# Performance work log

Measured on AMD Instinct MI355X. Metric: run time of the kernel, lower is better.

The kernel has to match this reference:

```python
import jax, jax.numpy as jnp
import numpy as np

N = 50000
E = 800000
F_IN = 128
H = 128
OUT = 2


def _init_linear(key, fan_in, fan_out):
    kw, kb = jax.random.split(key)
    bound = 1.0 / np.sqrt(fan_in)
    W = jax.random.uniform(kw, (fan_in, fan_out), jnp.float32, -bound, bound)
    b = jax.random.uniform(kb, (fan_out,), jnp.float32, -bound, bound)
    return W, b


def setup_inputs() -> dict:
    key = jax.random.key(0)
    ks = jax.random.split(key, 8)
    x = jax.random.normal(ks[0], (N, F_IN), jnp.float32)
    edge_index = jax.random.randint(ks[1], (2, E), 0, N, jnp.int64)
    # layer 0: in=F_IN -> out=H ; MLP([2*F_IN, H, H])
    w1_0, b1_0 = _init_linear(ks[2], 2 * F_IN, H)
    w2_0, b2_0 = _init_linear(ks[3], H, H)
    # layer 1: in=H -> out=H ; MLP([2*H, H, H])
    w1_1, b1_1 = _init_linear(ks[4], 2 * H, H)
    w2_1, b2_1 = _init_linear(ks[5], H, H)
    # layer 2 (last): in=H -> out=OUT ; MLP([2*H, OUT, OUT])
    w1_2, b1_2 = _init_linear(ks[6], 2 * H, OUT)
    w2_2, b2_2 = _init_linear(ks[7], OUT, OUT)
    return {"x": x, "edge_index": edge_index,
            "w1_0": w1_0, "b1_0": b1_0, "w2_0": w2_0, "b2_0": b2_0,
            "w1_1": w1_1, "b1_1": b1_1, "w2_1": w2_1, "b2_1": b2_1,
            "w1_2": w1_2, "b1_2": b1_2, "w2_2": w2_2, "b2_2": b2_2}


def _edge_conv(x, src, dst, W1, b1, W2, b2):
    # message on edge (j->i): MLP(concat[x_i, x_j - x_i]); max-aggregate at i
    xi = x[dst]                       # [E, F]
    xj = x[src]                       # [E, F]
    feat = jnp.concatenate([xi, xj - xi], axis=-1)   # [E, 2F]
    msg = jnp.maximum(feat @ W1 + b1, 0.0) @ W2 + b2  # [E, out]
    agg = jax.ops.segment_max(msg, dst, num_segments=N)
    # nodes with no incoming edges get 0 (PyG scatter-max convention)
    return jnp.where(jnp.isneginf(agg), 0.0, agg)


def reference(x, edge_index, w1_0, b1_0, w2_0, b2_0,
              w1_1, b1_1, w2_1, b2_1, w1_2, b1_2, w2_2, b2_2):
    src = edge_index[0]
    dst = edge_index[1]
    h = _edge_conv(x, src, dst, w1_0, b1_0, w2_0, b2_0)
    h = jnp.maximum(h, 0.0)  # inter-layer ReLU (dropout skipped: eval mode)
    h = _edge_conv(h, src, dst, w1_1, b1_1, w2_1, b2_1)
    h = jnp.maximum(h, 0.0)
    out = _edge_conv(h, src, dst, w1_2, b1_2, w2_2, b2_2)  # [N, 2]
    return out
```

## Files before the change

kernel.cpp:

```cpp
#include <hip/hip_runtime.h>
#include <cstdint>
#include <cstddef>


#define KEY_NEGINF 0x007FFFFFu

typedef __attribute__((ext_vector_type(8))) short bf16x8;
typedef __attribute__((ext_vector_type(4))) float f32x4;

__device__ __forceinline__ unsigned fkey(float f) {
  unsigned u = __float_as_uint(f);
  return (u & 0x80000000u) ? ~u : (u | 0x80000000u);
}
__device__ __forceinline__ float funkey(unsigned k) {
  unsigned u = (k & 0x80000000u) ? (k & 0x7FFFFFFFu) : ~k;
  return __uint_as_float(u);
}
__device__ __forceinline__ unsigned short f2bf(float f) {
  unsigned u = __float_as_uint(f);
  unsigned r = u + 0x7FFFu + ((u >> 16) & 1u);
  return (unsigned short)(r >> 16);
}
__device__ __forceinline__ float bflo(unsigned u) { return __uint_as_float(u << 16); }
__device__ __forceinline__ float bfhi(unsigned u) { return __uint_as_float(u & 0xFFFF0000u); }
__device__ __forceinline__ unsigned pack2(unsigned a, unsigned b) {
  float lo = fmaxf(bflo(a) + bflo(b), 0.f);
  float hi = fmaxf(bfhi(a) + bfhi(b), 0.f);
  return (unsigned)f2bf(lo) | ((unsigned)f2bf(hi) << 16);
}

__global__ void build_wcat(const float* __restrict__ w1, float* __restrict__ wcat,
                           int F, int O) {
  int i = blockIdx.x * 256 + threadIdx.x;
  int total = F * O;
  if (i >= total) return;
  int k = i / O, o = i - k * O;
  float wa = w1[(size_t)k * O + o];
  float wb = w1[(size_t)(F + k) * O + o];
  wcat[(size_t)k * 2 * O + o] = wa - wb;
  wcat[(size_t)k * 2 * O + O + o] = wb;
}

__global__ void fill_u32(unsigned* __restrict__ p, unsigned v, size_t n) {
  size_t i = (size_t)blockIdx.x * blockDim.x + threadIdx.x;
  size_t stride = (size_t)gridDim.x * blockDim.x;
  for (; i < n; i += stride) p[i] = v;
}

__global__ void decode_relu(unsigned* __restrict__ p, size_t n) {
  size_t i = (size_t)blockIdx.x * blockDim.x + threadIdx.x;
  size_t stride = (size_t)gridDim.x * blockDim.x;
  float* pf = reinterpret_cast<float*>(p);
  for (; i < n; i += stride) {
    float v = funkey(p[i]);
    pf[i] = fmaxf(v, 0.0f);
  }
}

__global__ void final_out(const unsigned* __restrict__ p, float* __restrict__ out, size_t n) {
  size_t i = (size_t)blockIdx.x * blockDim.x + threadIdx.x;
  size_t stride = (size_t)gridDim.x * blockDim.x;
  for (; i < n; i += stride) {
    unsigned k = p[i];
    out[i] = (k == KEY_NEGINF) ? 0.0f : funkey(k);
  }
}

__global__ __launch_bounds__(256, 2) void node_gemm(
    const float* __restrict__ hin, const float* __restrict__ wcat,
    const float* __restrict__ bias, unsigned short* __restrict__ Abf,
    unsigned short* __restrict__ Bbf, int nNodes) {
  __shared__ float xt[64][132];
  __shared__ float wt[32][256];
  int t = threadIdx.x;
  int m_base = blockIdx.x * 64;

  {
    int r = t >> 2, q = t & 3;
    int gm = m_base + r;
    const float4* src = reinterpret_cast<const float4*>(hin + (size_t)gm * 128);
    #pragma unroll
    for (int j = 0; j < 8; ++j) {
      int c4 = q + 4 * j;
      float4 v = make_float4(0.f, 0.f, 0.f, 0.f);
      if (gm < nNodes) v = src[c4];
      *reinterpret_cast<float4*>(&xt[r][c4 * 4]) = v;
    }
  }

  float acc[8][8];
  #pragma unroll
  for (int i = 0; i < 8; ++i)
    #pragma unroll
    for (int j = 0; j < 8; ++j) acc[i][j] = 0.f;

  int m0 = (t >> 5) * 8;
  int c0 = (t & 31) * 8;

  for (int kc = 0; kc < 128; kc += 32) {
    __syncthreads();
    #pragma unroll
    for (int j = 0; j < 8; ++j) {
      int idx = t + 256 * j;
      reinterpret_cast<float4*>(&wt[0][0])[idx] =
          reinterpret_cast<const float4*>(wcat + (size_t)kc * 256)[idx];
    }
    __syncthreads();
    #pragma unroll 4
    for (int k = 0; k < 32; ++k) {
      float xv[8];
      #pragma unroll
      for (int i = 0; i < 8; ++i) xv[i] = xt[m0 + i][kc + k];
      float4 w0 = *reinterpret_cast<float4*>(&wt[k][c0]);
      float4 w1 = *reinterpret_cast<float4*>(&wt[k][c0 + 4]);
      #pragma unroll
      for (int i = 0; i < 8; ++i) {
        acc[i][0] += xv[i] * w0.x; acc[i][1] += xv[i] * w0.y;
        acc[i][2] += xv[i] * w0.z; acc[i][3] += xv[i] * w0.w;
        acc[i][4] += xv[i] * w1.x; acc[i][5] += xv[i] * w1.y;
        acc[i][6] += xv[i] * w1.z; acc[i][7] += xv[i] * w1.w;
      }
    }
  }

  bool isA = (c0 < 128);
  float bv[8];
  #pragma unroll
  for (int j = 0; j < 8; ++j) bv[j] = isA ? bias[c0 + j] : 0.f;
  #pragma unroll
  for (int i = 0; i < 8; ++i) {
    int gm = m_base + m0 + i;
    if (gm >= nNodes) continue;
    alignas(16) unsigned short ob[8];
    #pragma unroll
    for (int j = 0; j < 8; ++j) ob[j] = f2bf(acc[i][j] + bv[j]);
    unsigned short* dst = isA ? (Abf + (size_t)gm * 128 + c0)
                              : (Bbf + (size_t)gm * 128 + (c0 - 128));
    *reinterpret_cast<uint4*>(dst) = *reinterpret_cast<const uint4*>(ob);
  }
}

__global__ __launch_bounds__(256, 3) void edge_mfma(
    const unsigned short* __restrict__ Abf, const unsigned short* __restrict__ Bbf,
    const int* __restrict__ ei,
    const float* __restrict__ W2, const float* __restrict__ b2,
    unsigned* __restrict__ aggk, int E_) {
  __shared__ unsigned short hs[64 * 128];
  __shared__ unsigned short wl[128 * 128];
  __shared__ int dstl[64];
  int t = threadIdx.x;
  int e_base = blockIdx.x * 64;

  if (t < 64) dstl[t] = ei[E_ + min(e_base + t, E_ - 1)];

  {
    int r = t >> 2, q = t & 3;
    int e = min(e_base + r, E_ - 1);
    int s = ei[e];
    int d = ei[E_ + e];
    const uint4* Ar = reinterpret_cast<const uint4*>(Abf + (size_t)d * 128);
    const uint4* Br = reinterpret_cast<const uint4*>(Bbf + (size_t)s * 128);
    #pragma unroll
    for (int j = 0; j < 4; ++j) {
      int c = q + 4 * j;
      uint4 a = Ar[c], b = Br[c];
      uint4 o;
      o.x = pack2(a.x, b.x);
      o.y = pack2(a.y, b.y);
      o.z = pack2(a.z, b.z);
      o.w = pack2(a.w, b.w);
      *reinterpret_cast<uint4*>(&hs[r * 128 + ((c ^ (r & 7)) * 8)]) = o;
    }
  }
  {
    for (int ci = t; ci < 2048; ci += 256) {
      int n = ci & 127, kc = ci >> 7;
      alignas(16) unsigned short tmp[8];
      #pragma unroll
      for (int j = 0; j < 8; ++j)
        tmp[j] = f2bf(W2[(size_t)(kc * 8 + j) * 128 + n]);
      *reinterpret_cast<uint4*>(&wl[n * 128 + ((kc ^ (n & 7)) * 8)]) =
          *reinterpret_cast<const uint4*>(tmp);
    }
  }
  __syncthreads();

  int l = t & 63;
  int w = t >> 6;
  int strip = w * 16;
  int lr = l & 15, lh = l >> 4;
  int erow = strip + lh * 4;

  unsigned cur[8][4];
  #pragma unroll
  for (int nt = 0; nt < 8; ++nt) {
    int col = nt * 16 + lr;
    #pragma unroll
    for (int j = 0; j < 4; ++j)
      cur[nt][j] = aggk[(size_t)dstl[erow + j] * 128 + col];
  }

  bf16x8 af[4];
  int arow = strip + lr;
  #pragma unroll
  for (int ks = 0; ks < 4; ++ks) {
    int c = ks * 4 + lh;
    af[ks] = *reinterpret_cast<const bf16x8*>(&hs[arow * 128 + ((c ^ (arow & 7)) * 8)]);
  }

  f32x4 acc[8];
  #pragma unroll
  for (int nt = 0; nt < 8; ++nt) {
    acc[nt] = (f32x4){0.f, 0.f, 0.f, 0.f};
    int n = nt * 16 + lr;
    #pragma unroll
    for (int ks = 0; ks < 4; ++ks) {
      int c = ks * 4 + lh;
      bf16x8 bf = *reinterpret_cast<const bf16x8*>(&wl[n * 128 + ((c ^ (n & 7)) * 8)]);
      acc[nt] = __builtin_amdgcn_mfma_f32_16x16x32_bf16(af[ks], bf, acc[nt], 0, 0, 0);
    }
  }

  #pragma unroll
  for (int nt = 0; nt < 8; ++nt) {
    int col = nt * 16 + lr;
    float bb = b2[col];
    #pragma unroll
    for (int j = 0; j < 4; ++j) {
      unsigned key = fkey(acc[nt][j] + bb);
      if (key > cur[nt][j])
        atomicMax(aggk + (size_t)dstl[erow + j] * 128 + col, key);
    }
  }
}

__global__ void node_thin(const float* __restrict__ hin, const float* __restrict__ wcat2,
                          const float* __restrict__ b1, float* __restrict__ AB2,
                          int nNodes) {
  __shared__ float w[128 * 4];
  int t = threadIdx.x;
  if (t < 128) *reinterpret_cast<float4*>(&w[t * 4]) =
      reinterpret_cast<const float4*>(wcat2)[t];
  __syncthreads();
  int node = blockIdx.x * 64 + (t >> 2);
  int o = t & 3;
  if (node >= nNodes) return;
  const float4* h4 = reinterpret_cast<const float4*>(hin + (size_t)node * 128);
  float acc = 0.f;
  #pragma unroll 8
  for (int kk = 0; kk < 32; ++kk) {
    float4 x = h4[kk];
    acc += x.x * w[(kk * 4 + 0) * 4 + o];
    acc += x.y * w[(kk * 4 + 1) * 4 + o];
    acc += x.z * w[(kk * 4 + 2) * 4 + o];
    acc += x.w * w[(kk * 4 + 3) * 4 + o];
  }
  if (o < 2) acc += b1[o];
  AB2[(size_t)node * 4 + o] = acc;
}

__global__ void edge_small(const float* __restrict__ AB2, const int* __restrict__ ei,
                           const float* __restrict__ w2, const float* __restrict__ b2,
                           unsigned* __restrict__ aggk2, int E_) {
  int e = blockIdx.x * 256 + threadIdx.x;
  if (e >= E_) return;
  int s = ei[e];
  int d = ei[E_ + e];
  float2 a = *reinterpret_cast<const float2*>(AB2 + (size_t)d * 4);
  float2 b = *reinterpret_cast<const float2*>(AB2 + (size_t)s * 4 + 2);
  float h0 = fmaxf(a.x + b.x, 0.f);
  float h1 = fmaxf(a.y + b.y, 0.f);
  float m0 = h0 * w2[0] + h1 * w2[2] + b2[0];
  float m1 = h0 * w2[1] + h1 * w2[3] + b2[1];
  atomicMax(aggk2 + (size_t)d * 2 + 0, fkey(m0));
  atomicMax(aggk2 + (size_t)d * 2 + 1, fkey(m1));
}

extern "C" void kernel_launch(void* const* d_in, const int* in_sizes, int n_in,
                              void* d_out, int out_size, void* d_ws, size_t ws_size,
                              hipStream_t stream) {
  const float* x    = (const float*)d_in[0];
  const int*   ei   = (const int*)d_in[1];
  const float* w1_0 = (const float*)d_in[2];
  const float* b1_0 = (const float*)d_in[3];
  const float* w2_0 = (const float*)d_in[4];
  const float* b2_0 = (const float*)d_in[5];
  const float* w1_1 = (const float*)d_in[6];
  const float* b1_1 = (const float*)d_in[7];
  const float* w2_1 = (const float*)d_in[8];
  const float* b2_1 = (const float*)d_in[9];
  const float* w1_2 = (const float*)d_in[10];
  const float* b1_2 = (const float*)d_in[11];
  const float* w2_2 = (const float*)d_in[12];
  const float* b2_2 = (const float*)d_in[13];

  const int N = in_sizes[0] / 128;
  const int E = in_sizes[1] / 2;

  char* ws = (char*)d_ws;
  const size_t NB = (size_t)N * 128 * 4;
  const size_t HB = (size_t)N * 128 * 2;
  unsigned*       Z    = (unsigned*)(ws);
  unsigned short* Abf  = (unsigned short*)(ws + NB);
  unsigned short* Bbf  = (unsigned short*)(ws + NB + HB);
  float*    AB2  = (float*)(ws + NB + 2 * HB);
  unsigned* agg2 = (unsigned*)(ws + NB + 2 * HB + (size_t)N * 16);
  float*    wc0  = (float*)(ws + NB + 2 * HB + (size_t)N * 16 + (size_t)N * 8);
  float*    wc1  = wc0 + 128 * 256;
  float*    wc2  = wc1 + 128 * 256;

  const int nb = (N + 63) / 64;
  const int eb = (E + 63) / 64;
  const size_t nH = (size_t)N * 128;

  build_wcat<<<64, 256, 0, stream>>>(w1_0, wc0, 128, 128);
  build_wcat<<<64, 256, 0, stream>>>(w1_1, wc1, 128, 128);
  build_wcat<<<1, 256, 0, stream>>>(w1_2, wc2, 128, 2);

  node_gemm<<<nb, 256, 0, stream>>>(x, wc0, b1_0, Abf, Bbf, N);
  fill_u32<<<1024, 256, 0, stream>>>(Z, KEY_NEGINF, nH);
  edge_mfma<<<eb, 256, 0, stream>>>(Abf, Bbf, ei, w2_0, b2_0, Z, E);
  decode_relu<<<1024, 256, 0, stream>>>(Z, nH);

  node_gemm<<<nb, 256, 0, stream>>>((const float*)Z, wc1, b1_1, Abf, Bbf, N);
  fill_u32<<<1024, 256, 0, stream>>>(Z, KEY_NEGINF, nH);
  edge_mfma<<<eb, 256, 0, stream>>>(Abf, Bbf, ei, w2_1, b2_1, Z, E);
  decode_relu<<<1024, 256, 0, stream>>>(Z, nH);

  node_thin<<<nb, 256, 0, stream>>>((const float*)Z, wc2, b1_2, AB2, N);
  fill_u32<<<256, 256, 0, stream>>>(agg2, KEY_NEGINF, (size_t)N * 2);
  edge_small<<<(E + 255) / 256, 256, 0, stream>>>(AB2, ei, w2_2, b2_2, agg2, E);
  final_out<<<((size_t)N * 2 + 255) / 256, 256, 0, stream>>>(agg2, (float*)d_out, (size_t)N * 2);
}
```

Measured before the change: 865.3 us.

## Use MFMA node GEMM, persistent prefetching edge kernel, fold decode into consumers

The FP32 node GEMM is replaced with a bf16 MFMA kernel whose weights are pre-converted and pre-swizzled once. The decode_relu passes are removed: the node kernels now decode the order-preserving keys and apply ReLU as they load. The edge kernel becomes persistent over a capped grid. It prefetches the next tile's gathered rows into registers while the current tile computes, and it loads W2 already in bf16 instead of converting it in every block. The aim is less FP32 ALU time, fewer full-array passes and fewer per-block weight conversions, at the cost of bf16 rounding on the node GEMM inputs and more register pressure in the edge kernel.

```diff
diff --git a/kernel.cpp b/kernel.cpp
--- a/kernel.cpp
+++ b/kernel.cpp
@@ -27,6 +27,34 @@
   float lo = fmaxf(bflo(a) + bflo(b), 0.f);
   float hi = fmaxf(bfhi(a) + bfhi(b), 0.f);
   return (unsigned)f2bf(lo) | ((unsigned)f2bf(hi) << 16);
+}
+
+__global__ void build_wcatbf(const float* __restrict__ w1, unsigned short* __restrict__ wcg) {
+  int i = blockIdx.x * 256 + threadIdx.x;
+  if (i >= 256 * 16) return;
+  int n = i >> 4, c = i & 15;
+  alignas(16) unsigned short ob[8];
+  #pragma unroll
+  for (int j = 0; j < 8; ++j) {
+    int k = c * 8 + j;
+    float v;
+    if (n < 128) v = w1[(size_t)k * 128 + n] - w1[(size_t)(128 + k) * 128 + n];
+    else         v = w1[(size_t)(128 + k) * 128 + (n - 128)];
+    ob[j] = f2bf(v);
+  }
+  *reinterpret_cast<uint4*>(&wcg[n * 128 + ((c ^ (n & 7)) * 8)]) =
+      *reinterpret_cast<const uint4*>(ob);
+}
+
+__global__ void build_w2bf(const float* __restrict__ w2, unsigned short* __restrict__ wlg) {
+  int i = blockIdx.x * 256 + threadIdx.x;
+  if (i >= 128 * 16) return;
+  int n = i >> 4, c = i & 15;
+  alignas(16) unsigned short ob[8];
+  #pragma unroll
+  for (int j = 0; j < 8; ++j) ob[j] = f2bf(w2[(size_t)(c * 8 + j) * 128 + n]);
+  *reinterpret_cast<uint4*>(&wlg[n * 128 + ((c ^ (n & 7)) * 8)]) =
+      *reinterpret_cast<const uint4*>(ob);
 }
 
 __global__ void build_wcat(const float* __restrict__ w1, float* __restrict__ wcat,
@@ -47,16 +75,6 @@
   for (; i < n; i += stride) p[i] = v;
 }
 
-__global__ void decode_relu(unsigned* __restrict__ p, size_t n) {
-  size_t i = (size_t)blockIdx.x * blockDim.x + threadIdx.x;
-  size_t stride = (size_t)gridDim.x * blockDim.x;
-  float* pf = reinterpret_cast<float*>(p);
-  for (; i < n; i += stride) {
-    float v = funkey(p[i]);
-    pf[i] = fmaxf(v, 0.0f);
-  }
-}
-
 __global__ void final_out(const unsigned* __restrict__ p, float* __restrict__ out, size_t n) {
   size_t i = (size_t)blockIdx.x * blockDim.x + threadIdx.x;
   size_t stride = (size_t)gridDim.x * blockDim.x;
@@ -66,175 +84,173 @@
   }
 }
 
-__global__ __launch_bounds__(256, 2) void node_gemm(
-    const float* __restrict__ hin, const float* __restrict__ wcat,
-    const float* __restrict__ bias, unsigned short* __restrict__ Abf,
-    unsigned short* __restrict__ Bbf, int nNodes) {
-  __shared__ float xt[64][132];
-  __shared__ float wt[32][256];
+__global__ __launch_bounds__(256, 2) void node_mfma(
+    const unsigned* __restrict__ hin, int decode,
+    const unsigned short* __restrict__ wcg, const float* __restrict__ b1,
+    unsigned short* __restrict__ Abf, unsigned short* __restrict__ Bbf, int nN) {
+  __shared__ unsigned short at[64 * 128];
+  __shared__ unsigned short wt[256 * 128];
   int t = threadIdx.x;
+  {
+    const uint4* src = reinterpret_cast<const uint4*>(wcg);
+    uint4* dst = reinterpret_cast<uint4*>(wt);
+    for (int i = t; i < 4096; i += 256) dst[i] = src[i];
+  }
   int m_base = blockIdx.x * 64;
-
   {
     int r = t >> 2, q = t & 3;
-    int gm = m_base + r;
-    const float4* src = reinterpret_cast<const float4*>(hin + (size_t)gm * 128);
-    #pragma unroll
-    for (int j = 0; j < 8; ++j) {
-      int c4 = q + 4 * j;
-      float4 v = make_float4(0.f, 0.f, 0.f, 0.f);
-      if (gm < nNodes) v = src[c4];
-      *reinterpret_cast<float4*>(&xt[r][c4 * 4]) = v;
-    }
-  }
-
-  float acc[8][8];
-  #pragma unroll
-  for (int i = 0; i < 8; ++i)
-    #pragma unroll
-    for (int j = 0; j < 8; ++j) acc[i][j] = 0.f;
-
-  int m0 = (t >> 5) * 8;
-  int c0 = (t & 31) * 8;
-
-  for (int kc = 0; kc < 128; kc += 32) {
-    __syncthreads();
-    #pragma unroll
-    for (int j = 0; j < 8; ++j) {
-      int idx = t + 256 * j;
-      reinterpret_cast<float4*>(&wt[0][0])[idx] =
-          reinterpret_cast<const float4*>(wcat + (size_t)kc * 256)[idx];
-    }
-    __syncthreads();
-    #pragma unroll 4
-    for (int k = 0; k < 32; ++k) {
-      float xv[8];
-      #pragma unroll
-      for (int i = 0; i < 8; ++i) xv[i] = xt[m0 + i][kc + k];
-      float4 w0 = *reinterpret_cast<float4*>(&wt[k][c0]);
-      float4 w1 = *reinterpret_cast<float4*>(&wt[k][c0 + 4]);
-      #pragma unroll
-      for (int i = 0; i < 8; ++i) {
-        acc[i][0] += xv[i] * w0.x; acc[i][1] += xv[i] * w0.y;
-        acc[i][2] += xv[i] * w0.z; acc[i][3] += xv[i] * w0.w;
-        acc[i][4] += xv[i] * w1.x; acc[i][5] += xv[i] * w1.y;
-        acc[i][6] += xv[i] * w1.z; acc[i][7] += xv[i] * w1.w;
+    int gm = min(m_base + r, nN - 1);
+    const uint4* src = reinterpret_cast<const uint4*>(hin + (size_t)gm * 128);
+    #pragma unroll
+    for (int j = 0; j < 4; ++j) {
+      int c = q + 4 * j;
+      uint4 u0 = src[c * 2], u1 = src[c * 2 + 1];
+      unsigned b[8] = {u0.x, u0.y, u0.z, u0.w, u1.x, u1.y, u1.z, u1.w};
+      alignas(16) unsigned short ob[8];
+      #pragma unroll
+      for (int e = 0; e < 8; ++e) {
+        float v = decode ? fmaxf(funkey(b[e]), 0.f) : __uint_as_float(b[e]);
+        ob[e] = f2bf(v);
       }
-    }
-  }
-
-  bool isA = (c0 < 128);
-  float bv[8];
-  #pragma unroll
-  for (int j = 0; j < 8; ++j) bv[j] = isA ? bias[c0 + j] : 0.f;
-  #pragma unroll
-  for (int i = 0; i < 8; ++i) {
-    int gm = m_base + m0 + i;
-    if (gm >= nNodes) continue;
-    alignas(16) unsigned short ob[8];
-    #pragma unroll
-    for (int j = 0; j < 8; ++j) ob[j] = f2bf(acc[i][j] + bv[j]);
-    unsigned short* dst = isA ? (Abf + (size_t)gm * 128 + c0)
-                              : (Bbf + (size_t)gm * 128 + (c0 - 128));
-    *reinterpret_cast<uint4*>(dst) = *reinterpret_cast<const uint4*>(ob);
+      *reinterpret_cast<uint4*>(&at[r * 128 + ((c ^ (r & 7)) * 8)]) =
+          *reinterpret_cast<const uint4*>(ob);
+    }
+  }
+  __syncthreads();
+
+  int l = t & 63, w = t >> 6;
+  int strip = w * 16, lr = l & 15, lh = l >> 4;
+  int arow = strip + lr, erow = strip + lh * 4;
+
+  bf16x8 af[4];
+  #pragma unroll
+  for (int ks = 0; ks < 4; ++ks)
+    af[ks] = *reinterpret_cast<const bf16x8*>(
+        &at[arow * 128 + (((ks * 4 + lh) ^ (arow & 7)) * 8)]);
+
+  #pragma unroll
+  for (int nt = 0; nt < 16; ++nt) {
+    f32x4 acc = (f32x4){0.f, 0.f, 0.f, 0.f};
+    int n = nt * 16 + lr;
+    #pragma unroll
+    for (int ks = 0; ks < 4; ++ks) {
+      bf16x8 bf = *reinterpret_cast<const bf16x8*>(
+          &wt[n * 128 + (((ks * 4 + lh) ^ (n & 7)) * 8)]);
+      acc = __builtin_amdgcn_mfma_f32_16x16x32_bf16(af[ks], bf, acc, 0, 0, 0);
+    }
+    bool isA = (n < 128);
+    float bias = isA ? b1[n] : 0.f;
+    int coln = isA ? n : n - 128;
+    unsigned short* plane = isA ? Abf : Bbf;
+    #pragma unroll
+    for (int j = 0; j < 4; ++j) {
+      int gm = m_base + erow + j;
+      if (gm < nN) plane[(size_t)gm * 128 + coln] = f2bf(acc[j] + bias);
+    }
   }
 }
 
 __global__ __launch_bounds__(256, 3) void edge_mfma(
     const unsigned short* __restrict__ Abf, const unsigned short* __restrict__ Bbf,
-    const int* __restrict__ ei,
-    const float* __restrict__ W2, const float* __restrict__ b2,
-    unsigned* __restrict__ aggk, int E_) {
+    const int* __restrict__ ei, const unsigned short* __restrict__ wlg,
+    const float* __restrict__ b2, unsigned* __restrict__ aggk, int E_) {
   __shared__ unsigned short hs[64 * 128];
   __shared__ unsigned short wl[128 * 128];
   __shared__ int dstl[64];
   int t = threadIdx.x;
-  int e_base = blockIdx.x * 64;
-
-  if (t < 64) dstl[t] = ei[E_ + min(e_base + t, E_ - 1)];
-
   {
-    int r = t >> 2, q = t & 3;
-    int e = min(e_base + r, E_ - 1);
-    int s = ei[e];
-    int d = ei[E_ + e];
+    const uint4* src = reinterpret_cast<const uint4*>(wlg);
+    uint4* dst = reinterpret_cast<uint4*>(wl);
+    for (int i = t; i < 2048; i += 256) dst[i] = src[i];
+  }
+  int l = t & 63, w = t >> 6;
+  int strip = w * 16, lr = l & 15, lh = l >> 4;
+  int arow = strip + lr, erow = strip + lh * 4;
+  int r = t >> 2, q = t & 3;
+
+  float bb[8];
+  #pragma unroll
+  for (int nt = 0; nt < 8; ++nt) bb[nt] = b2[nt * 16 + lr];
+
+  int ntiles = (E_ + 63) >> 6;
+  int tile = blockIdx.x;
+  uint4 ga[4], gb[4];
+  int nd = 0;
+  if (tile < ntiles) {
+    int e = min(tile * 64 + r, E_ - 1);
+    int s = ei[e], d = ei[E_ + e];
     const uint4* Ar = reinterpret_cast<const uint4*>(Abf + (size_t)d * 128);
     const uint4* Br = reinterpret_cast<const uint4*>(Bbf + (size_t)s * 128);
     #pragma unroll
+    for (int j = 0; j < 4; ++j) { ga[j] = Ar[q + 4 * j]; gb[j] = Br[q + 4 * j]; }
+    nd = ei[E_ + min(tile * 64 + t, E_ - 1)];
+  }
+
+  for (; tile < ntiles; tile += gridDim.x) {
+    __syncthreads();
+    #pragma unroll
     for (int j = 0; j < 4; ++j) {
       int c = q + 4 * j;
-      uint4 a = Ar[c], b = Br[c];
       uint4 o;
-      o.x = pack2(a.x, b.x);
-      o.y = pack2(a.y, b.y);
-      o.z = pack2(a.z, b.z);
-      o.w = pack2(a.w, b.w);
+      o.x = pack2(ga[j].x, gb[j].x);
+      o.y = pack2(ga[j].y, gb[j].y);
+      o.z = pack2(ga[j].z, gb[j].z);
+      o.w = pack2(ga[j].w, gb[j].w);
       *reinterpret_cast<uint4*>(&hs[r * 128 + ((c ^ (r & 7)) * 8)]) = o;
     }
-  }
-  {
-    for (int ci = t; ci < 2048; ci += 256) {
-      int n = ci & 127, kc = ci >> 7;
-      alignas(16) unsigned short tmp[8];
-      #pragma unroll
-      for (int j = 0; j < 8; ++j)
-        tmp[j] = f2bf(W2[(size_t)(kc * 8 + j) * 128 + n]);
-      *reinterpret_cast<uint4*>(&wl[n * 128 + ((kc ^ (n & 7)) * 8)]) =
-          *reinterpret_cast<const uint4*>(tmp);
-    }
-  }
-  __syncthreads();
-
-  int l = t & 63;
-  int w = t >> 6;
-  int strip = w * 16;
-  int lr = l & 15, lh = l >> 4;
-  int erow = strip + lh * 4;
-
-  unsigned cur[8][4];
-  #pragma unroll
-  for (int nt = 0; nt < 8; ++nt) {
-    int col = nt * 16 + lr;
-    #pragma unroll
-    for (int j = 0; j < 4; ++j)
-      cur[nt][j] = aggk[(size_t)dstl[erow + j] * 128 + col];
-  }
-
-  bf16x8 af[4];
-  int arow = strip + lr;
-  #pragma unroll
-  for (int ks = 0; ks < 4; ++ks) {
-    int c = ks * 4 + lh;
-    af[ks] = *reinterpret_cast<const bf16x8*>(&hs[arow * 128 + ((c ^ (arow & 7)) * 8)]);
-  }
-
-  f32x4 acc[8];
-  #pragma unroll
-  for (int nt = 0; nt < 8; ++nt) {
-    acc[nt] = (f32x4){0.f, 0.f, 0.f, 0.f};
-    int n = nt * 16 + lr;
-    #pragma unroll
-    for (int ks = 0; ks < 4; ++ks) {
-      int c = ks * 4 + lh;
-      bf16x8 bf = *reinterpret_cast<const bf16x8*>(&wl[n * 128 + ((c ^ (n & 7)) * 8)]);
-      acc[nt] = __builtin_amdgcn_mfma_f32_16x16x32_bf16(af[ks], bf, acc[nt], 0, 0, 0);
-    }
-  }
-
-  #pragma unroll
-  for (int nt = 0; nt < 8; ++nt) {
-    int col = nt * 16 + lr;
-    float bb = b2[col];
-    #pragma unroll
-    for (int j = 0; j < 4; ++j) {
-      unsigned key = fkey(acc[nt][j] + bb);
-      if (key > cur[nt][j])
-        atomicMax(aggk + (size_t)dstl[erow + j] * 128 + col, key);
-    }
-  }
-}
-
-__global__ void node_thin(const float* __restrict__ hin, const float* __restrict__ wcat2,
+    if (t < 64) dstl[t] = nd;
+    __syncthreads();
+
+    int next = tile + gridDim.x;
+    if (next < ntiles) {
+      int e = min(next * 64 + r, E_ - 1);
+      int s = ei[e], d = ei[E_ + e];
+      const uint4* Ar = reinterpret_cast<const uint4*>(Abf + (size_t)d * 128);
+      const uint4* Br = reinterpret_cast<const uint4*>(Bbf + (size_t)s * 128);
+      #pragma unroll
+      for (int j = 0; j < 4; ++j) { ga[j] = Ar[q + 4 * j]; gb[j] = Br[q + 4 * j]; }
+      nd = ei[E_ + min(next * 64 + t, E_ - 1)];
+    }
+
+    int drow[4];
+    #pragma unroll
+    for (int j = 0; j < 4; ++j) drow[j] = dstl[erow + j];
+    unsigned cur[8][4];
+    #pragma unroll
+    for (int nt = 0; nt < 8; ++nt) {
+      int col = nt * 16 + lr;
+      #pragma unroll
+      for (int j = 0; j < 4; ++j)
+        cur[nt][j] = aggk[(size_t)drow[j] * 128 + col];
+    }
+
+    bf16x8 af[4];
+    #pragma unroll
+    for (int ks = 0; ks < 4; ++ks)
+      af[ks] = *reinterpret_cast<const bf16x8*>(
+          &hs[arow * 128 + (((ks * 4 + lh) ^ (arow & 7)) * 8)]);
+
+    #pragma unroll
+    for (int nt = 0; nt < 8; ++nt) {
+      f32x4 acc = (f32x4){0.f, 0.f, 0.f, 0.f};
+      int n = nt * 16 + lr;
+      #pragma unroll
+      for (int ks = 0; ks < 4; ++ks) {
+        bf16x8 bf = *reinterpret_cast<const bf16x8*>(
+            &wl[n * 128 + (((ks * 4 + lh) ^ (n & 7)) * 8)]);
+        acc = __builtin_amdgcn_mfma_f32_16x16x32_bf16(af[ks], bf, acc, 0, 0, 0);
+      }
+      #pragma unroll
+      for (int j = 0; j < 4; ++j) {
+        unsigned key = fkey(acc[j] + bb[nt]);
+        if (key > cur[nt][j])
+          atomicMax(aggk + (size_t)drow[j] * 128 + n, key);
+      }
+    }
+  }
+}
+
+__global__ void node_thin(const unsigned* __restrict__ hin, const float* __restrict__ wcat2,
                           const float* __restrict__ b1, float* __restrict__ AB2,
                           int nNodes) {
   __shared__ float w[128 * 4];
@@ -245,15 +261,15 @@
   int node = blockIdx.x * 64 + (t >> 2);
   int o = t & 3;
   if (node >= nNodes) return;
-  const float4* h4 = reinterpret_cast<const float4*>(hin + (size_t)node * 128);
+  const uint4* h4 = reinterpret_cast<const uint4*>(hin + (size_t)node * 128);
   float acc = 0.f;
   #pragma unroll 8
   for (int kk = 0; kk < 32; ++kk) {
-    float4 x = h4[kk];
-    acc += x.x * w[(kk * 4 + 0) * 4 + o];
-    acc += x.y * w[(kk * 4 + 1) * 4 + o];
-    acc += x.z * w[(kk * 4 + 2) * 4 + o];
-    acc += x.w * w[(kk * 4 + 3) * 4 + o];
+    uint4 x = h4[kk];
+    acc += fmaxf(funkey(x.x), 0.f) * w[(kk * 4 + 0) * 4 + o];
+    acc += fmaxf(funkey(x.y), 0.f) * w[(kk * 4 + 1) * 4 + o];
+    acc += fmaxf(funkey(x.z), 0.f) * w[(kk * 4 + 2) * 4 + o];
+    acc += fmaxf(funkey(x.w), 0.f) * w[(kk * 4 + 3) * 4 + o];
   }
   if (o < 2) acc += b1[o];
   AB2[(size_t)node * 4 + o] = acc;
@@ -305,29 +321,33 @@
   unsigned short* Bbf  = (unsigned short*)(ws + NB + HB);
   float*    AB2  = (float*)(ws + NB + 2 * HB);
   unsigned* agg2 = (unsigned*)(ws + NB + 2 * HB + (size_t)N * 16);
-  float*    wc0  = (float*)(ws + NB + 2 * HB + (size_t)N * 16 + (size_t)N * 8);
-  float*    wc1  = wc0 + 128 * 256;
-  float*    wc2  = wc1 + 128 * 256;
+  char*     wp   = ws + NB + 2 * HB + (size_t)N * 16 + (size_t)N * 8;
+  unsigned short* wcg0 = (unsigned short*)(wp);
+  unsigned short* wcg1 = (unsigned short*)(wp + 65536);
+  unsigned short* wlg0 = (unsigned short*)(wp + 131072);
+  unsigned short* wlg1 = (unsigned short*)(wp + 163840);
+  float*          wc2  = (float*)(wp + 196608);
 
   const int nb = (N + 63) / 64;
   const int eb = (E + 63) / 64;
+  const int egrid = eb < 768 ? eb : 768;
   const size_t nH = (size_t)N * 128;
 
-  build_wcat<<<64, 256, 0, stream>>>(w1_0, wc0, 128, 128);
-  build_wcat<<<64, 256, 0, stream>>>(w1_1, wc1, 128, 128);
+  build_wcatbf<<<16, 256, 0, stream>>>(w1_0, wcg0);
+  build_wcatbf<<<16, 256, 0, stream>>>(w1_1, wcg1);
+  build_w2bf<<<8, 256, 0, stream>>>(w2_0, wlg0);
+  build_w2bf<<<8, 256, 0, stream>>>(w2_1, wlg1);
   build_wcat<<<1, 256, 0, stream>>>(w1_2, wc2, 128, 2);
 
-  node_gemm<<<nb, 256, 0, stream>>>(x, wc0, b1_0, Abf, Bbf, N);
+  node_mfma<<<nb, 256, 0, stream>>>((const unsigned*)x, 0, wcg0, b1_0, Abf, Bbf, N);
   fill_u32<<<1024, 256, 0, stream>>>(Z, KEY_NEGINF, nH);
-  edge_mfma<<<eb, 256, 0, stream>>>(Abf, Bbf, ei, w2_0, b2_0, Z, E);
-  decode_relu<<<1024, 256, 0, stream>>>(Z, nH);
-
-  node_gemm<<<nb, 256, 0, stream>>>((const float*)Z, wc1, b1_1, Abf, Bbf, N);
+  edge_mfma<<<egrid, 256, 0, stream>>>(Abf, Bbf, ei, wlg0, b2_0, Z, E);
+
+  node_mfma<<<nb, 256, 0, stream>>>(Z, 1, wcg1, b1_1, Abf, Bbf, N);
   fill_u32<<<1024, 256, 0, stream>>>(Z, KEY_NEGINF, nH);
-  edge_mfma<<<eb, 256, 0, stream>>>(Abf, Bbf, ei, w2_1, b2_1, Z, E);
-  decode_relu<<<1024, 256, 0, stream>>>(Z, nH);
-
-  node_thin<<<nb, 256, 0, stream>>>((const float*)Z, wc2, b1_2, AB2, N);
+  edge_mfma<<<egrid, 256, 0, stream>>>(Abf, Bbf, ei, wlg1, b2_1, Z, E);
+
+  node_thin<<<nb, 256, 0, stream>>>(Z, wc2, b1_2, AB2, N);
   fill_u32<<<256, 256, 0, stream>>>(agg2, KEY_NEGINF, (size_t)N * 2);
   edge_small<<<(E + 255) / 256, 256, 0, stream>>>(AB2, ei, w2_2, b2_2, agg2, E);
   final_out<<<((size_t)N * 2 + 255) / 256, 256, 0, stream>>>(agg2, (float*)d_out, (size_t)N * 2);
```

Measured after the change: 734.2 us. -15.2%, faster.
